# Optimization experiments

Hardware: AMD Instinct MI355X
Metric: run time of the kernel (lower is better)

## Reference

```python
import math
import jax, jax.numpy as jnp
import numpy as np

B, T, C, H = 4, 2048, 1024, 16
D = C // H  # head dim = 64


def setup_inputs() -> dict:
    key = jax.random.key(0)
    ks = jax.random.split(key, 5)
    s = 1.0 / math.sqrt(C)
    return {
        "x": jax.random.normal(ks[0], (B, T, C), jnp.float32),
        "w_qkv": jax.random.normal(ks[1], (C, 3 * C), jnp.float32) * s,
        "b_qkv": jax.random.normal(ks[2], (3 * C,), jnp.float32) * 0.02,
        "w_out": jax.random.normal(ks[3], (C, C), jnp.float32) * s,
        "b_out": jax.random.normal(ks[4], (C,), jnp.float32) * 0.02,
    }


def reference(x, w_qkv, b_qkv, w_out, b_out):
    # qkv projection: (B,T,C) @ (C,3C) -> split into Q,K,V
    qkv = x @ w_qkv + b_qkv
    q, k, v = jnp.split(qkv, 3, axis=-1)
    # reshape to (B,H,T,D)
    q = q.reshape(B, T, H, D).transpose(0, 2, 1, 3)
    k = k.reshape(B, T, H, D).transpose(0, 2, 1, 3)
    v = v.reshape(B, T, H, D).transpose(0, 2, 1, 3)
    # scaled scores with causal mask
    scores = jnp.einsum("bhqd,bhkd->bhqk", q, k) * (1.0 / math.sqrt(D))
    causal = jnp.tril(jnp.ones((T, T), dtype=bool))
    scores = jnp.where(causal[None, None], scores, -jnp.inf)
    attn = jax.nn.softmax(scores, axis=-1)  # dropout_rate=0 (eval)
    out = jnp.einsum("bhqk,bhkd->bhqd", attn, v)
    out = out.transpose(0, 2, 1, 3).reshape(B, T, C)
    return out @ w_out + b_out
```

## Files before the change

### kernel.cpp

```cpp
#include <hip/hip_runtime.h>
#include <cstdint>
#include <cstddef>

typedef _Float16 h8_t __attribute__((ext_vector_type(8)));
typedef _Float16 h4_t __attribute__((ext_vector_type(4)));
typedef float f32x4 __attribute__((ext_vector_type(4)));
typedef float f32x16 __attribute__((ext_vector_type(16)));
typedef unsigned u32x4 __attribute__((ext_vector_type(4)));

#define MFMA_16x16x32_F16(a, b, c) __builtin_amdgcn_mfma_f32_16x16x32_f16(a, b, c, 0, 0, 0)
#define MFMA_32x32x16_F16(a, b, c) __builtin_amdgcn_mfma_f32_32x32x16_f16(a, b, c, 0, 0, 0)

__device__ inline void gload_lds16(const void* g, void* l) {
  __builtin_amdgcn_global_load_lds((const __attribute__((address_space(1))) void*)g,
                                   (__attribute__((address_space(3))) void*)l, 16, 0, 0);
}

#define CFENCE asm volatile("" ::: "memory")
#define RAW_BAR() do { CFENCE; __builtin_amdgcn_s_barrier(); CFENCE; } while (0)

__global__ void prep_kernel(const float* __restrict__ x, _Float16* __restrict__ x16,
                            const float* __restrict__ wqkv, _Float16* __restrict__ wqkvT,
                            const float* __restrict__ wout, _Float16* __restrict__ woutT) {
  int blk = blockIdx.x;
  if (blk < 8192) {
    int i = blk * 256 + threadIdx.x;
    float4 v = reinterpret_cast<const float4*>(x)[i];
    h4_t h;
    h[0] = (_Float16)v.x; h[1] = (_Float16)v.y; h[2] = (_Float16)v.z; h[3] = (_Float16)v.w;
    reinterpret_cast<h4_t*>(x16)[i] = h;
    return;
  }
  blk -= 8192;
  __shared__ float tile[32][33];
  const float* src;
  _Float16* dst;
  int Cc, cb, rb;
  if (blk < 3072) { src = wqkv; dst = wqkvT; Cc = 3072; cb = blk % 96; rb = blk / 96; }
  else { blk -= 3072; src = wout; dst = woutT; Cc = 1024; cb = blk & 31; rb = blk >> 5; }
  const int R = 1024;
  int tx = threadIdx.x & 31;
  int ty = threadIdx.x >> 5;
  int c0 = cb * 32, r0 = rb * 32;
#pragma unroll
  for (int i = 0; i < 4; ++i)
    tile[ty + i * 8][tx] = src[(size_t)(r0 + ty + i * 8) * Cc + (c0 + tx)];
  __syncthreads();
#pragma unroll
  for (int i = 0; i < 4; ++i)
    dst[(size_t)(c0 + ty + i * 8) * R + (r0 + tx)] = (_Float16)tile[tx][ty + i * 8];
}

__global__ __launch_bounds__(512, 2) void gemm_qkv_kernel(
    const _Float16* __restrict__ A, const _Float16* __restrict__ Bt,
    const float* __restrict__ bias, _Float16* __restrict__ outQ,
    _Float16* __restrict__ outK, _Float16* __restrict__ outV) {
  __shared__ _Float16 Al[3][8192];
  __shared__ _Float16 Bl[3][12288];

  const int tid = threadIdx.x;
  const int lane = tid & 63;
  const int w = tid >> 6;
  const int wm = w >> 2, wn = w & 3;
  const int bm = blockIdx.x >> 3;
  const int bn = blockIdx.x & 7;
  const int m0 = bm * 256;
  const int n0 = bn * 384;

  f32x4 acc[8][6];
#pragma unroll
  for (int i = 0; i < 8; ++i)
#pragma unroll
    for (int j = 0; j < 6; ++j) acc[i][j] = (f32x4){0.f, 0.f, 0.f, 0.f};

  const int fg0 = tid >> 6;
  const int sl = tid & 63;
  const int srow = fg0 * 16 + (sl & 15);
  const int scol = (sl >> 4) * 8;
  const _Float16* aS = A + (size_t)(m0 + srow) * 1024 + scol;
  const _Float16* bS = Bt + (size_t)(n0 + srow) * 1024 + scol;
  const int sdst = tid * 8;

  auto stageA = [&](int buf, int kt) {
    const int k0 = kt * 32;
    gload_lds16(aS + k0, &Al[buf][sdst]);
    gload_lds16(aS + 131072 + k0, &Al[buf][sdst + 4096]);
  };
  auto stageB = [&](int buf, int kt) {
    const int k0 = kt * 32;
    gload_lds16(bS + k0, &Bl[buf][sdst]);
    gload_lds16(bS + 131072 + k0, &Bl[buf][sdst + 4096]);
    gload_lds16(bS + 262144 + k0, &Bl[buf][sdst + 8192]);
  };

  const int offA0 = (wm * 8 * 64 + lane) * 8;
  const int offB0 = (wn * 6 * 64 + lane) * 8;

  stageA(0, 0); stageB(0, 0);
  stageA(1, 1); stageB(1, 1);
  asm volatile("s_waitcnt vmcnt(5)" ::: "memory");
  RAW_BAR();

  int cur = 0;
#pragma unroll 1
  for (int t = 0; t < 32; ++t) {
    int nb = cur + 2; if (nb >= 3) nb -= 3;
    const bool st = (t + 2) < 32;
    const _Float16* Ab = &Al[cur][0];
    const _Float16* Bb = &Bl[cur][0];
    h8_t af[4], bf[6];

#pragma unroll
    for (int mf = 0; mf < 4; ++mf) af[mf] = *(const h8_t*)&Ab[offA0 + mf * 512];
#pragma unroll
    for (int nf = 0; nf < 6; ++nf) bf[nf] = *(const h8_t*)&Bb[offB0 + nf * 512];
    if (st) stageA(nb, t + 2);
    RAW_BAR();
    asm volatile("s_waitcnt lgkmcnt(0)" ::: "memory");
    __builtin_amdgcn_sched_barrier(0);
    __builtin_amdgcn_s_setprio(1);
#pragma unroll
    for (int mf = 0; mf < 4; ++mf)
#pragma unroll
      for (int nf = 0; nf < 6; ++nf)
        acc[mf][nf] = MFMA_16x16x32_F16(af[mf], bf[nf], acc[mf][nf]);
    __builtin_amdgcn_s_setprio(0);
    RAW_BAR();

#pragma unroll
    for (int mf = 0; mf < 4; ++mf) af[mf] = *(const h8_t*)&Ab[offA0 + (4 + mf) * 512];
    if (st) stageB(nb, t + 2);
    RAW_BAR();
    asm volatile("s_waitcnt lgkmcnt(0)" ::: "memory");
    __builtin_amdgcn_sched_barrier(0);
    __builtin_amdgcn_s_setprio(1);
#pragma unroll
    for (int mf = 0; mf < 4; ++mf)
#pragma unroll
      for (int nf = 0; nf < 6; ++nf)
        acc[4 + mf][nf] = MFMA_16x16x32_F16(af[mf], bf[nf], acc[4 + mf][nf]);
    __builtin_amdgcn_s_setprio(0);
    if (t < 31) {
      if (st) asm volatile("s_waitcnt vmcnt(5)" ::: "memory");
      else asm volatile("s_waitcnt vmcnt(0)" ::: "memory");
      RAW_BAR();
    }
    ++cur; if (cur == 3) cur = 0;
  }

  const int gm0 = m0 + wm * 128;
  const int gn0 = n0 + wn * 96;
#pragma unroll
  for (int mf = 0; mf < 8; ++mf) {
#pragma unroll
    for (int nf = 0; nf < 6; ++nf) {
      const int gn = gn0 + nf * 16 + (lane & 15);
      const int tm0 = gm0 + mf * 16 + (lane >> 4) * 4;
      const float bv = bias[gn];
      const int which = gn >> 10;
      const int nn = gn & 1023;
      const int h = nn >> 6, d = nn & 63;
      const int t0 = tm0 & 2047, b = tm0 >> 11;
      const int bh = b * 16 + h;
      if (which == 2) {
        h4_t pack;
#pragma unroll
        for (int r = 0; r < 4; ++r) pack[r] = (_Float16)(acc[mf][nf][r] + bv);
        *reinterpret_cast<h4_t*>(&outV[((size_t)bh * 64 + d) * 2048 + t0]) = pack;
      } else {
        _Float16* dst = (which == 0) ? outQ : outK;
        const float scale = (which == 0) ? 0.18033688011112042f : 1.0f;
#pragma unroll
        for (int r = 0; r < 4; ++r)
          dst[((size_t)bh * 2048 + t0 + r) * 64 + d] = (_Float16)((acc[mf][nf][r] + bv) * scale);
      }
    }
  }
}

__global__ __launch_bounds__(256, 3) void gemm_out_kernel(
    const _Float16* __restrict__ A, const _Float16* __restrict__ Bt,
    const float* __restrict__ bias, float* __restrict__ outF, int NB) {
  __shared__ _Float16 Al[3][4096];
  __shared__ _Float16 Bl[3][4096];
  const int tid = threadIdx.x;
  const int lane = tid & 63;
  const int w = tid >> 6;
  const int bm = blockIdx.x / NB;
  const int bn = blockIdx.x % NB;
  const int wm = w & 1, wn = w >> 1;
  const int m0 = bm * 128, n0 = bn * 128;

  f32x4 acc[4][4];
#pragma unroll
  for (int m = 0; m < 4; ++m)
#pragma unroll
    for (int n = 0; n < 4; ++n) acc[m][n] = (f32x4){0.f, 0.f, 0.f, 0.f};

  const int seg0 = w * 2, seg1 = w * 2 + 1;
  const int r0s = seg0 * 16 + (lane >> 2);
  const int r1s = seg1 * 16 + (lane >> 2);
  const int c0s = ((lane & 3) ^ ((r0s >> 1) & 3)) * 8;
  const int c1s = ((lane & 3) ^ ((r1s >> 1) & 3)) * 8;
  const _Float16* aS0 = A + (size_t)(m0 + r0s) * 1024 + c0s;
  const _Float16* aS1 = A + (size_t)(m0 + r1s) * 1024 + c1s;
  const _Float16* bS0 = Bt + (size_t)(n0 + r0s) * 1024 + c0s;
  const _Float16* bS1 = Bt + (size_t)(n0 + r1s) * 1024 + c1s;
  const int d0 = seg0 * 512 + lane * 8;
  const int d1 = seg1 * 512 + lane * 8;

  auto stage = [&](int buf, int kt) {
    const int k0 = kt * 32;
    gload_lds16(aS0 + k0, &Al[buf][d0]);
    gload_lds16(bS0 + k0, &Bl[buf][d0]);
    gload_lds16(aS1 + k0, &Al[buf][d1]);
    gload_lds16(bS1 + k0, &Bl[buf][d1]);
  };

  int offA[4], offB[4];
#pragma unroll
  for (int i = 0; i < 4; ++i) {
    const int rowA = wm * 64 + i * 16 + (lane & 15);
    offA[i] = rowA * 32 + (((lane >> 4) ^ ((rowA >> 1) & 3)) * 8);
    const int rowB = wn * 64 + i * 16 + (lane & 15);
    offB[i] = rowB * 32 + (((lane >> 4) ^ ((rowB >> 1) & 3)) * 8);
  }

  stage(0, 0);
  stage(1, 1);
  asm volatile("s_waitcnt vmcnt(4)" ::: "memory");
  RAW_BAR();

  int cur = 0;
#pragma unroll 1
  for (int t = 0; t < 32; ++t) {
    int nb = cur + 2; if (nb >= 3) nb -= 3;
    if (t + 2 < 32) stage(nb, t + 2);
    const _Float16* Ab = &Al[cur][0];
    const _Float16* Bb = &Bl[cur][0];
    h8_t af[4], bf[4];
#pragma unroll
    for (int i = 0; i < 4; ++i) af[i] = *(const h8_t*)&Ab[offA[i]];
#pragma unroll
    for (int j = 0; j < 4; ++j) bf[j] = *(const h8_t*)&Bb[offB[j]];
#pragma unroll
    for (int i = 0; i < 4; ++i)
#pragma unroll
      for (int j = 0; j < 4; ++j)
        acc[i][j] = MFMA_16x16x32_F16(af[i], bf[j], acc[i][j]);
    if (t < 31) {
      if (t + 2 < 32) asm volatile("s_waitcnt vmcnt(4)" ::: "memory");
      else asm volatile("s_waitcnt vmcnt(0)" ::: "memory");
      RAW_BAR();
    }
    ++cur; if (cur == 3) cur = 0;
  }

  const int gm0 = bm * 128 + wm * 64;
  const int gn0 = bn * 128 + wn * 64;
#pragma unroll
  for (int i = 0; i < 4; ++i) {
#pragma unroll
    for (int j = 0; j < 4; ++j) {
      const int gn = gn0 + j * 16 + (lane & 15);
      const int tm0 = gm0 + i * 16 + (lane >> 4) * 4;
      const float bv = bias[gn];
#pragma unroll
      for (int r = 0; r < 4; ++r)
        outF[(size_t)(tm0 + r) * 1024 + gn] = acc[i][j][r] + bv;
    }
  }
}

__device__ inline void stage_kv64(const _Float16* __restrict__ Kbh, const _Float16* __restrict__ Vbh,
                                  int kt, _Float16* Kd, _Float16* Vd, int w, int lane) {
  const _Float16* Kg = Kbh + (size_t)kt * 64 * 64;
  const _Float16* Vg = Vbh + kt * 64;
#pragma unroll
  for (int c = 0; c < 2; ++c) {
    const int idx = (2 * w + c) * 64 + lane;
    const int row = idx >> 3;
    const int chs = (idx & 7) ^ (row & 7);
    gload_lds16(Kg + row * 64 + chs * 8, Kd + idx * 8);
    gload_lds16(Vg + (size_t)row * 2048 + chs * 8, Vd + idx * 8);
  }
}

__device__ inline void pack_pfrag(const float* e, h8_t* out) {
  unsigned u[8];
#pragma unroll
  for (int i = 0; i < 8; ++i) {
    auto hv = __builtin_amdgcn_cvt_pkrtz(e[2 * i], e[2 * i + 1]);
    u[i] = __builtin_bit_cast(unsigned, hv);
  }
  auto r02 = __builtin_amdgcn_permlane32_swap(u[0], u[2], false, false);
  auto r13 = __builtin_amdgcn_permlane32_swap(u[1], u[3], false, false);
  auto r46 = __builtin_amdgcn_permlane32_swap(u[4], u[6], false, false);
  auto r57 = __builtin_amdgcn_permlane32_swap(u[5], u[7], false, false);
  u32x4 w0 = {(unsigned)r02[0], (unsigned)r13[0], (unsigned)r02[1], (unsigned)r13[1]};
  u32x4 w1 = {(unsigned)r46[0], (unsigned)r57[0], (unsigned)r46[1], (unsigned)r57[1]};
  out[0] = __builtin_bit_cast(h8_t, w0);
  out[1] = __builtin_bit_cast(h8_t, w1);
}

__global__ __launch_bounds__(256, 2) void attn_kernel(
    const _Float16* __restrict__ Q, const _Float16* __restrict__ K,
    const _Float16* __restrict__ Vt, _Float16* __restrict__ O) {
  __shared__ _Float16 Kl[2][2][64 * 64];
  __shared__ _Float16 Vl[2][2][64 * 64];
  const int tid = threadIdx.x;
  const int lane = tid & 63;
  const int w = tid >> 6;
  const int hi = lane >> 5;
  const int l31 = lane & 31;
  const int bh = blockIdx.x & 63;
  const int pr = blockIdx.x >> 6;
  const int b = bh >> 4, h = bh & 15;
  const _Float16* Kbh = K + (size_t)bh * 2048 * 64;
  const _Float16* Vbh = Vt + (size_t)bh * 64 * 2048;

#pragma unroll
  for (int gi = 0; gi < 2; ++gi) {
    const int g = gi ? (15 - pr) : pr;
    const int nT = g + 1;
    const int qbase = g * 128 + w * 32;
    const int qrow = qbase + l31;

    h8_t qf[4];
    const _Float16* Qp = Q + ((size_t)bh * 2048 + qrow) * 64 + hi * 8;
#pragma unroll
    for (int ds = 0; ds < 4; ++ds)
      qf[ds] = *reinterpret_cast<const h8_t*>(Qp + ds * 16);

    f32x16 oa[2] = {};
    float m = -1e30f, lsum = 0.f;

    stage_kv64(Kbh, Vbh, 0, &Kl[0][0][0], &Vl[0][0][0], w, lane);
    stage_kv64(Kbh, Vbh, 1, &Kl[0][1][0], &Vl[0][1][0], w, lane);
    __syncthreads();

#pragma unroll 1
    for (int T = 0; T < nT; ++T) {
      const int cur = T & 1;
      if (T + 1 < nT) {
        stage_kv64(Kbh, Vbh, 2 * (T + 1), &Kl[cur ^ 1][0][0], &Vl[cur ^ 1][0][0], w, lane);
        stage_kv64(Kbh, Vbh, 2 * (T + 1) + 1, &Kl[cur ^ 1][1][0], &Vl[cur ^ 1][1][0], w, lane);
      }

      const bool diag = (T == g);
      const bool skip1 = diag && (w < 2);
      f32x16 s[2][2];

      __builtin_amdgcn_s_setprio(1);
#pragma unroll
      for (int half = 0; half < 2; ++half) {
        if (half == 1 && skip1) {
#pragma unroll
          for (int r = 0; r < 16; ++r) { s[1][0][r] = -1e30f; s[1][1][r] = -1e30f; }
        } else {
          const char* Kb = (const char*)&Kl[cur][half][0];
          f32x16 a0 = {}, a1 = {};
#pragma unroll
          for (int ds = 0; ds < 4; ++ds) {
            const int bc = ds * 32 + hi * 16;
            h8_t kf0 = *(const h8_t*)(Kb + l31 * 128 + (bc ^ ((l31 & 7) << 4)));
            h8_t kf1 = *(const h8_t*)(Kb + (32 + l31) * 128 + (bc ^ ((l31 & 7) << 4)));
            a0 = MFMA_32x32x16_F16(kf0, qf[ds], a0);
            a1 = MFMA_32x32x16_F16(kf1, qf[ds], a1);
          }
          s[half][0] = a0;
          s[half][1] = a1;
        }
      }
      __builtin_amdgcn_s_setprio(0);
      if (diag) {
#pragma unroll
        for (int half = 0; half < 2; ++half) {
          if (half == 1 && skip1) continue;
#pragma unroll
          for (int r = 0; r < 16; ++r) {
            const int kr = T * 128 + half * 64 + (r & 3) + 8 * (r >> 2) + 4 * hi;
            if (kr > qrow) s[half][0][r] = -1e30f;
            if (kr + 32 > qrow) s[half][1][r] = -1e30f;
          }
        }
      }

      float t[16];
#pragma unroll
      for (int r = 0; r < 16; ++r)
        t[r] = fmaxf(fmaxf(s[0][0][r], s[0][1][r]), fmaxf(s[1][0][r], s[1][1][r]));
#pragma unroll
      for (int st = 8; st >= 1; st >>= 1)
#pragma unroll
        for (int r = 0; r < st; ++r) t[r] = fmaxf(t[r], t[r + st]);
      const float pmax = fmaxf(t[0], __shfl_xor(t[0], 32));
      const float mnew = fmaxf(m, pmax);
      if (__any(mnew > m + 8.f)) {
        const float al = __builtin_amdgcn_exp2f(m - mnew);
        lsum *= al;
#pragma unroll
        for (int r = 0; r < 16; ++r) { oa[0][r] *= al; oa[1][r] *= al; }
        m = mnew;
      }
      float ps = 0.f;
#pragma unroll
      for (int half = 0; half < 2; ++half)
#pragma unroll
        for (int sub = 0; sub < 2; ++sub)
#pragma unroll
          for (int r = 0; r < 16; ++r) {
            const float pv = __builtin_amdgcn_exp2f(s[half][sub][r] - m);
            s[half][sub][r] = pv;
            ps += pv;
          }
      ps += __shfl_xor(ps, 32);
      lsum += ps;

#pragma unroll
      for (int half = 0; half < 2; ++half) {
        if (half == 1 && skip1) continue;
        h8_t pf[4];
        pack_pfrag((const float*)&s[half][0], pf + 0);
        pack_pfrag((const float*)&s[half][1], pf + 2);
        const char* Vb = (const char*)&Vl[cur][half][0];
        __builtin_amdgcn_s_setprio(1);
#pragma unroll
        for (int dt = 0; dt < 2; ++dt) {
#pragma unroll
          for (int kg = 0; kg < 4; ++kg) {
            const int row = dt * 32 + l31;
            const int bc = kg * 32 + hi * 16;
            h8_t vf = *(const h8_t*)(Vb + row * 128 + (bc ^ ((row & 7) << 4)));
            oa[dt] = MFMA_32x32x16_F16(vf, pf[kg], oa[dt]);
          }
        }
        __builtin_amdgcn_s_setprio(0);
      }
      __syncthreads();
    }

    const float inv = __builtin_amdgcn_rcpf(lsum);
    _Float16* Op = O + ((size_t)b * 2048 + qrow) * 1024 + h * 64;
#pragma unroll
    for (int dt = 0; dt < 2; ++dt) {
#pragma unroll
      for (int rg = 0; rg < 4; ++rg) {
        h4_t pk4;
#pragma unroll
        for (int i = 0; i < 4; ++i) pk4[i] = (_Float16)(oa[dt][rg * 4 + i] * inv);
        *reinterpret_cast<h4_t*>(Op + dt * 32 + rg * 8 + hi * 4) = pk4;
      }
    }
  }
}

extern "C" void kernel_launch(void* const* d_in, const int* in_sizes, int n_in,
                              void* d_out, int out_size, void* d_ws, size_t ws_size,
                              hipStream_t stream) {
  (void)in_sizes; (void)n_in; (void)out_size; (void)ws_size;
  const float* x = (const float*)d_in[0];
  const float* w_qkv = (const float*)d_in[1];
  const float* b_qkv = (const float*)d_in[2];
  const float* w_out = (const float*)d_in[3];
  const float* b_out = (const float*)d_in[4];
  float* out = (float*)d_out;

  char* ws = (char*)d_ws;
  size_t off = 0;
  auto alloc = [&](size_t bytes) {
    void* p = ws + off;
    off += (bytes + 255) & ~(size_t)255;
    return p;
  };
  _Float16* x16 = (_Float16*)alloc((size_t)8192 * 1024 * 2);
  _Float16* wqkvT = (_Float16*)alloc((size_t)3072 * 1024 * 2);
  _Float16* woutT = (_Float16*)alloc((size_t)1024 * 1024 * 2);
  _Float16* Qh = (_Float16*)alloc((size_t)64 * 2048 * 64 * 2);
  _Float16* Kh = (_Float16*)alloc((size_t)64 * 2048 * 64 * 2);
  _Float16* Vth = (_Float16*)alloc((size_t)64 * 64 * 2048 * 2);
  _Float16* Oh = (_Float16*)alloc((size_t)8192 * 1024 * 2);

  prep_kernel<<<8192 + 3072 + 1024, 256, 0, stream>>>(x, x16, w_qkv, wqkvT, w_out, woutT);
  gemm_qkv_kernel<<<256, 512, 0, stream>>>(x16, wqkvT, b_qkv, Qh, Kh, Vth);
  attn_kernel<<<64 * 8, 256, 0, stream>>>(Qh, Kh, Vth, Oh);
  gemm_out_kernel<<<64 * 8, 256, 0, stream>>>(Oh, woutT, b_out, out, 8);
}
```

Measured before the change: 169.1 us.

## Halve QKV GEMM M-tile, double K-step, switch to double-buffered LDS pipeline

The QKV projection GEMM tile shrinks from 256x384 to 128x384 and the K step grows from 32 to 64, which doubles the grid to 512 blocks. The triple-buffered LDS ring becomes a double buffer, with the B-tile staging split into two halves issued alongside the two MFMA phases. Only one barrier per K iteration remains. The aim is fewer synchronisations and more blocks to spread across CUs. In exchange, each B tile is reloaded by twice as many blocks, the larger B buffer raises LDS use, and the full vmcnt(0) wait each iteration exposes more global load latency.

```diff
diff --git a/kernel.cpp b/kernel.cpp
--- a/kernel.cpp
+++ b/kernel.cpp
@@ -55,8 +55,8 @@
     const _Float16* __restrict__ A, const _Float16* __restrict__ Bt,
     const float* __restrict__ bias, _Float16* __restrict__ outQ,
     _Float16* __restrict__ outK, _Float16* __restrict__ outV) {
-  __shared__ _Float16 Al[3][8192];
-  __shared__ _Float16 Bl[3][12288];
+  __shared__ _Float16 Al[2][8192];
+  __shared__ _Float16 Bl[2][24576];
 
   const int tid = threadIdx.x;
   const int lane = tid & 63;
@@ -64,58 +64,60 @@
   const int wm = w >> 2, wn = w & 3;
   const int bm = blockIdx.x >> 3;
   const int bn = blockIdx.x & 7;
-  const int m0 = bm * 256;
+  const int m0 = bm * 128;
   const int n0 = bn * 384;
 
-  f32x4 acc[8][6];
-#pragma unroll
-  for (int i = 0; i < 8; ++i)
+  f32x4 acc[4][6];
+#pragma unroll
+  for (int i = 0; i < 4; ++i)
 #pragma unroll
     for (int j = 0; j < 6; ++j) acc[i][j] = (f32x4){0.f, 0.f, 0.f, 0.f};
 
-  const int fg0 = tid >> 6;
-  const int sl = tid & 63;
-  const int srow = fg0 * 16 + (sl & 15);
-  const int scol = (sl >> 4) * 8;
+  const int sg2 = tid >> 6;
+  const int srow = (sg2 >> 1) * 16 + (lane & 15);
+  const int scol = (sg2 & 1) * 32 + (lane >> 4) * 8;
   const _Float16* aS = A + (size_t)(m0 + srow) * 1024 + scol;
   const _Float16* bS = Bt + (size_t)(n0 + srow) * 1024 + scol;
   const int sdst = tid * 8;
 
   auto stageA = [&](int buf, int kt) {
-    const int k0 = kt * 32;
+    const int k0 = kt * 64;
     gload_lds16(aS + k0, &Al[buf][sdst]);
-    gload_lds16(aS + 131072 + k0, &Al[buf][sdst + 4096]);
+    gload_lds16(aS + (size_t)64 * 1024 + k0, &Al[buf][sdst + 4096]);
   };
-  auto stageB = [&](int buf, int kt) {
-    const int k0 = kt * 32;
+  auto stageB1 = [&](int buf, int kt) {
+    const int k0 = kt * 64;
     gload_lds16(bS + k0, &Bl[buf][sdst]);
-    gload_lds16(bS + 131072 + k0, &Bl[buf][sdst + 4096]);
-    gload_lds16(bS + 262144 + k0, &Bl[buf][sdst + 8192]);
+    gload_lds16(bS + (size_t)64 * 1024 + k0, &Bl[buf][sdst + 4096]);
+    gload_lds16(bS + (size_t)128 * 1024 + k0, &Bl[buf][sdst + 8192]);
   };
-
-  const int offA0 = (wm * 8 * 64 + lane) * 8;
-  const int offB0 = (wn * 6 * 64 + lane) * 8;
-
-  stageA(0, 0); stageB(0, 0);
-  stageA(1, 1); stageB(1, 1);
-  asm volatile("s_waitcnt vmcnt(5)" ::: "memory");
+  auto stageB2 = [&](int buf, int kt) {
+    const int k0 = kt * 64;
+    gload_lds16(bS + (size_t)192 * 1024 + k0, &Bl[buf][sdst + 12288]);
+    gload_lds16(bS + (size_t)256 * 1024 + k0, &Bl[buf][sdst + 16384]);
+    gload_lds16(bS + (size_t)320 * 1024 + k0, &Bl[buf][sdst + 20480]);
+  };
+
+  const int offA0 = (wm * 4 * 2) * 512 + lane * 8;
+  const int offB0 = (wn * 6 * 2) * 512 + lane * 8;
+
+  stageA(0, 0); stageB1(0, 0); stageB2(0, 0);
+  asm volatile("s_waitcnt vmcnt(0)" ::: "memory");
   RAW_BAR();
 
-  int cur = 0;
 #pragma unroll 1
-  for (int t = 0; t < 32; ++t) {
-    int nb = cur + 2; if (nb >= 3) nb -= 3;
-    const bool st = (t + 2) < 32;
-    const _Float16* Ab = &Al[cur][0];
-    const _Float16* Bb = &Bl[cur][0];
+  for (int t = 0; t < 16; ++t) {
+    const int buf = t & 1;
+    const bool st = (t + 1) < 16;
+    const _Float16* Ab = &Al[buf][0];
+    const _Float16* Bb = &Bl[buf][0];
     h8_t af[4], bf[6];
 
 #pragma unroll
-    for (int mf = 0; mf < 4; ++mf) af[mf] = *(const h8_t*)&Ab[offA0 + mf * 512];
-#pragma unroll
-    for (int nf = 0; nf < 6; ++nf) bf[nf] = *(const h8_t*)&Bb[offB0 + nf * 512];
-    if (st) stageA(nb, t + 2);
-    RAW_BAR();
+    for (int mf = 0; mf < 4; ++mf) af[mf] = *(const h8_t*)&Ab[offA0 + (mf * 2 + 0) * 512];
+#pragma unroll
+    for (int nf = 0; nf < 6; ++nf) bf[nf] = *(const h8_t*)&Bb[offB0 + (nf * 2 + 0) * 512];
+    if (st) { stageA(buf ^ 1, t + 1); stageB1(buf ^ 1, t + 1); }
     asm volatile("s_waitcnt lgkmcnt(0)" ::: "memory");
     __builtin_amdgcn_sched_barrier(0);
     __builtin_amdgcn_s_setprio(1);
@@ -125,12 +127,12 @@
       for (int nf = 0; nf < 6; ++nf)
         acc[mf][nf] = MFMA_16x16x32_F16(af[mf], bf[nf], acc[mf][nf]);
     __builtin_amdgcn_s_setprio(0);
-    RAW_BAR();
-
-#pragma unroll
-    for (int mf = 0; mf < 4; ++mf) af[mf] = *(const h8_t*)&Ab[offA0 + (4 + mf) * 512];
-    if (st) stageB(nb, t + 2);
-    RAW_BAR();
+
+#pragma unroll
+    for (int mf = 0; mf < 4; ++mf) af[mf] = *(const h8_t*)&Ab[offA0 + (mf * 2 + 1) * 512];
+#pragma unroll
+    for (int nf = 0; nf < 6; ++nf) bf[nf] = *(const h8_t*)&Bb[offB0 + (nf * 2 + 1) * 512];
+    if (st) stageB2(buf ^ 1, t + 1);
     asm volatile("s_waitcnt lgkmcnt(0)" ::: "memory");
     __builtin_amdgcn_sched_barrier(0);
     __builtin_amdgcn_s_setprio(1);
@@ -138,20 +140,19 @@
     for (int mf = 0; mf < 4; ++mf)
 #pragma unroll
       for (int nf = 0; nf < 6; ++nf)
-        acc[4 + mf][nf] = MFMA_16x16x32_F16(af[mf], bf[nf], acc[4 + mf][nf]);
+        acc[mf][nf] = MFMA_16x16x32_F16(af[mf], bf[nf], acc[mf][nf]);
     __builtin_amdgcn_s_setprio(0);
-    if (t < 31) {
-      if (st) asm volatile("s_waitcnt vmcnt(5)" ::: "memory");
-      else asm volatile("s_waitcnt vmcnt(0)" ::: "memory");
+
+    if (st) {
+      asm volatile("s_waitcnt vmcnt(0)" ::: "memory");
       RAW_BAR();
     }
-    ++cur; if (cur == 3) cur = 0;
-  }
-
-  const int gm0 = m0 + wm * 128;
+  }
+
+  const int gm0 = m0 + wm * 64;
   const int gn0 = n0 + wn * 96;
 #pragma unroll
-  for (int mf = 0; mf < 8; ++mf) {
+  for (int mf = 0; mf < 4; ++mf) {
 #pragma unroll
     for (int nf = 0; nf < 6; ++nf) {
       const int gn = gn0 + nf * 16 + (lane & 15);
@@ -482,7 +483,7 @@
   _Float16* Oh = (_Float16*)alloc((size_t)8192 * 1024 * 2);
 
   prep_kernel<<<8192 + 3072 + 1024, 256, 0, stream>>>(x, x16, w_qkv, wqkvT, w_out, woutT);
-  gemm_qkv_kernel<<<256, 512, 0, stream>>>(x16, wqkvT, b_qkv, Qh, Kh, Vth);
+  gemm_qkv_kernel<<<512, 512, 0, stream>>>(x16, wqkvT, b_qkv, Qh, Kh, Vth);
   attn_kernel<<<64 * 8, 256, 0, stream>>>(Qh, Kh, Vth, Oh);
   gemm_out_kernel<<<64 * 8, 256, 0, stream>>>(Oh, woutT, b_out, out, 8);
 }
```

Measured after the change: 188.0 us. 11.1% more time.
